# Kernel tuning notes

Measured on AMD Instinct MI355X. Metric: run time of the kernel, lower is better.

## Reference

```python
import jax, jax.numpy as jnp
import numpy as np

B, M, C, D, FF, FEAT = 1, 1024, 128, 512, 1024, 20
PAIR = 3 * D + 2 * FEAT  # slow_scorer_size = 1576


def _ffnn(x, W0, b0, W1, b1):
    # FFNN(depth=1): hidden relu layer then linear output (eval mode, no dropout)
    return jax.nn.relu(x @ W0 + b0) @ W1 + b1


def _batch_gather(x, idx):
    # x: [B, M, ...], idx: [B, ...] int -> gather along mention dim per batch
    return jax.vmap(lambda xb, ib: xb[ib])(x, idx)


def _bucket_distance(d):
    # log-scale distance buckets 0..9 (identity for d<=4)
    log_idx = jnp.floor(jnp.log(jnp.maximum(d, 1).astype(jnp.float32)) / jnp.log(2.0)).astype(jnp.int32) + 3
    return jnp.clip(jnp.where(d <= 4, d, log_idx), 0, 9)


def setup_inputs() -> dict:
    key = jax.random.key(0)
    ks = jax.random.split(key, 10)
    s = 0.02
    return {
        'mention_emb': jax.random.normal(ks[0], (B, M, D), dtype=jnp.float32),
        'mention_cluster_ids': jax.random.randint(ks[1], (B, M), 0, 200),
        'mention_speaker_ids': jax.random.randint(ks[2], (B, M), 0, 2),
        'ms_W0': jax.random.normal(ks[3], (D, FF), dtype=jnp.float32) * s,
        'ms_b0': jnp.zeros((FF,), jnp.float32),
        'ms_W1': jax.random.normal(ks[4], (FF, 1), dtype=jnp.float32) * s,
        'ms_b1': jnp.zeros((1,), jnp.float32),
        'sp_W0': jax.random.normal(ks[5], (PAIR, FF), dtype=jnp.float32) * s,
        'sp_b0': jnp.zeros((FF,), jnp.float32),
        'sp_W1': jax.random.normal(ks[6], (FF, 1), dtype=jnp.float32) * s,
        'sp_b1': jnp.zeros((1,), jnp.float32),
        'speaker_emb': jax.random.normal(ks[7], (2, FEAT), dtype=jnp.float32) * s,
        'bucket_emb': jax.random.normal(ks[8], (10, FEAT), dtype=jnp.float32) * s,
    }


def reference(mention_emb, mention_cluster_ids, mention_speaker_ids,
              ms_W0, ms_b0, ms_W1, ms_b1,
              sp_W0, sp_b0, sp_W1, sp_b1,
              speaker_emb, bucket_emb):
    # mention scoring
    mention_scores = _ffnn(mention_emb, ms_W0, ms_b0, ms_W1, ms_b1)[..., 0]  # [B, M]

    # get_antecedent_info: fixed window of C previous mentions
    offsets = jnp.arange(1, C + 1)[None, None, :]                    # [1,1,C]
    raw = jnp.arange(M)[None, :, None] - offsets                      # [1,M,C]
    antecedents = jnp.broadcast_to(jnp.clip(raw, 0, M - 1), (B, M, C))
    ant_mask = jnp.broadcast_to(raw >= 0, (B, M, C))

    fast_scores = _batch_gather(mention_scores, antecedents) + mention_scores[:, :, None]
    antecedent_emb = _batch_gather(mention_emb, antecedents)          # [B,M,C,D]

    # slow pair scorer features
    same_speaker = (_batch_gather(mention_speaker_ids, antecedents) == mention_speaker_ids[:, :, None]).astype(jnp.int32)
    speaker_feat = speaker_emb[same_speaker]                          # [B,M,C,FEAT]
    bucket_feat = jnp.broadcast_to(bucket_emb[_bucket_distance(offsets)], (B, M, C, FEAT))

    src = jnp.broadcast_to(mention_emb[:, :, None, :], (B, M, C, D))
    pair_emb = jnp.concatenate([src, antecedent_emb, src * antecedent_emb, speaker_feat, bucket_feat], axis=-1)
    slow_scores = _ffnn(pair_emb, sp_W0, sp_b0, sp_W1, sp_b1)[..., 0]  # [B,M,C]

    antecedent_scores = fast_scores + slow_scores + jnp.log(ant_mask.astype(jnp.float32))
    overall_scores = jnp.concatenate([jnp.zeros((B, M, 1), jnp.float32), antecedent_scores], axis=2)
    overall_dist = jax.nn.softmax(overall_scores, axis=-1)
    eps = 1e-6
    overall_dist = jnp.clip(overall_dist, eps, 1.0 - eps)
    overall_dist = overall_dist / jnp.sum(overall_dist, axis=-1, keepdims=True)

    # coref loss from cluster ids
    ant_cluster = _batch_gather(mention_cluster_ids, antecedents) * ant_mask.astype(mention_cluster_ids.dtype)
    same_cluster = ant_cluster == mention_cluster_ids[:, :, None]
    non_dummy = (mention_cluster_ids > 0)[:, :, None]
    ant_labels = same_cluster & non_dummy
    dummy_labels = ~jnp.any(ant_labels, axis=2, keepdims=True)
    overall_labels = jnp.concatenate([dummy_labels, ant_labels], axis=2)
    loss = -jnp.sum(jnp.log(overall_dist) * overall_labels.astype(jnp.float32), axis=2)
    loss = jnp.mean(jnp.sum(loss, axis=1))
    return overall_dist, loss
```

## Files before the change

kernel.cpp:

```cpp
#include <hip/hip_runtime.h>
#include <math.h>

#define MM 1024
#define DD 512
#define CC 128
#define LDSR 516


typedef __attribute__((ext_vector_type(8))) short bf16x8;
typedef __attribute__((ext_vector_type(4), aligned(8))) short bf16x4a;
typedef __attribute__((ext_vector_type(4))) float f32x4;
typedef __attribute__((ext_vector_type(16))) float f32x16;

__device__ __forceinline__ ushort bf16_rn(float x) {
    uint u = __float_as_uint(x);
    uint r = u + 0x7fffu + ((u >> 16) & 1u);
    return (ushort)(r >> 16);
}
__device__ __forceinline__ float bf16_to_f(ushort u) {
    return __uint_as_float(((uint)u) << 16);
}
__device__ __forceinline__ bf16x8 ld_lds16(const ushort* p) {
    bf16x4a lo = *(const bf16x4a*)p;
    bf16x4a hi = *(const bf16x4a*)(p + 4);
    return __builtin_shufflevector(lo, hi, 0, 1, 2, 3, 4, 5, 6, 7);
}

__global__ __launch_bounds__(256) void prep_emb(const float* __restrict__ emb,
                                                ushort* __restrict__ embb)
{
    int i = blockIdx.x * 256 + threadIdx.x;
    float2 v = ((const float2*)emb)[i];
    ushort2 o;
    o.x = bf16_rn(v.x);
    o.y = bf16_rn(v.y);
    ((ushort2*)embb)[i] = o;
}

__global__ __launch_bounds__(256) void prep_wall(const float* __restrict__ ms_W0,
                                                 const float* __restrict__ sp_W0,
                                                 ushort* __restrict__ Wall)
{
    __shared__ float t[64][65];
    const int k0 = blockIdx.x * 64;
    const int n0 = blockIdx.y * 64;
    const int g = n0 >> 10;
    const float* src = (g == 0) ? ms_W0 : (sp_W0 + (size_t)(g - 1) * 512 * 1024);
    const int col0 = n0 & 1023;
    const int tr = threadIdx.x >> 6, tc = threadIdx.x & 63;
#pragma unroll
    for (int i = 0; i < 16; ++i) {
        int k = tr + i * 4;
        t[k][tc] = src[(size_t)(k0 + k) * 1024 + col0 + tc];
    }
    __syncthreads();
    const int f = threadIdx.x >> 2;
    const int c4 = threadIdx.x & 3;
    ushort tmp[16];
#pragma unroll
    for (int j = 0; j < 16; ++j) tmp[j] = bf16_rn(t[c4 * 16 + j][f]);
    uint4* dst = (uint4*)(Wall + (size_t)(n0 + f) * 512 + k0 + c4 * 16);
    dst[0] = *(uint4*)&tmp[0];
    dst[1] = *(uint4*)&tmp[8];
}

__global__ __launch_bounds__(64) void prep_wfrag(const float* __restrict__ sp_W0,
                                                 ushort* __restrict__ Wfrag)
{
    const int ts = blockIdx.x;
    const int l = threadIdx.x;
    const int tt = ts >> 5, s = ts & 31;
    const int f = tt * 32 + (l & 31);
    const int kb = s * 16 + (l >> 5) * 8;
    const float* W = sp_W0 + (size_t)1024 * 1024;
    ushort tmp[8];
#pragma unroll
    for (int j = 0; j < 8; ++j) tmp[j] = bf16_rn(W[(size_t)(kb + j) * 1024 + f]);
    uint4* dst = (uint4*)(Wfrag + ((size_t)ts * 64 + l) * 8);
    *dst = *(uint4*)&tmp[0];
}

__global__ __launch_bounds__(256) void gemm_h_mfma(
    const ushort* __restrict__ embb, const ushort* __restrict__ Wall,
    float* __restrict__ H)
{
    const int n0 = blockIdx.x * 128;
    const int m0 = blockIdx.y * 128;
    const int lane = threadIdx.x & 63, wave = threadIdx.x >> 6;
    const int wx = wave & 1, wy = wave >> 1;
    const int l15 = lane & 15, lq = lane >> 4;

    const ushort* arow[4];
#pragma unroll
    for (int mi = 0; mi < 4; ++mi)
        arow[mi] = embb + (size_t)(m0 + wy * 64 + mi * 16 + l15) * 512;
    const ushort* brow[4];
#pragma unroll
    for (int ni = 0; ni < 4; ++ni)
        brow[ni] = Wall + (size_t)(n0 + wx * 64 + ni * 16 + l15) * 512;

    f32x4 acc[4][4];
#pragma unroll
    for (int i = 0; i < 4; ++i)
#pragma unroll
        for (int j = 0; j < 4; ++j) acc[i][j] = (f32x4)0.f;

    for (int kt = 0; kt < 512; kt += 32) {
        const int ko = kt + lq * 8;
        bf16x8 av[4], bv[4];
#pragma unroll
        for (int mi = 0; mi < 4; ++mi) av[mi] = *(const bf16x8*)(arow[mi] + ko);
#pragma unroll
        for (int ni = 0; ni < 4; ++ni) bv[ni] = *(const bf16x8*)(brow[ni] + ko);
#pragma unroll
        for (int mi = 0; mi < 4; ++mi)
#pragma unroll
            for (int ni = 0; ni < 4; ++ni)
                acc[mi][ni] = __builtin_amdgcn_mfma_f32_16x16x32_bf16(av[mi], bv[ni], acc[mi][ni], 0, 0, 0);
    }
#pragma unroll
    for (int mi = 0; mi < 4; ++mi)
#pragma unroll
        for (int r = 0; r < 4; ++r) {
            int mrow = m0 + wy * 64 + mi * 16 + lq * 4 + r;
#pragma unroll
            for (int ni = 0; ni < 4; ++ni)
                H[(size_t)mrow * 3072 + n0 + wx * 64 + ni * 16 + l15] = acc[mi][ni][r];
        }
}

__global__ void small_proj(const float* __restrict__ speaker_emb,
                           const float* __restrict__ bucket_emb,
                           const float* __restrict__ sp_W0,
                           float* __restrict__ spk_proj, float* __restrict__ bkt_proj)
{
    int r = blockIdx.x;
    const float* e; const float* W; float* out;
    if (r < 2) { e = speaker_emb + r * 20; W = sp_W0 + (size_t)1536 * 1024; out = spk_proj + r * 1024; }
    else       { e = bucket_emb + (r - 2) * 20; W = sp_W0 + (size_t)1556 * 1024; out = bkt_proj + (r - 2) * 1024; }
    float ek[20];
#pragma unroll
    for (int k = 0; k < 20; ++k) ek[k] = e[k];
    for (int f = threadIdx.x; f < 1024; f += blockDim.x) {
        float s = 0.f;
#pragma unroll
        for (int k = 0; k < 20; ++k) s = fmaf(ek[k], W[(size_t)k * 1024 + f], s);
        out[f] = s;
    }
}

__global__ __launch_bounds__(256) void mention_score(
    const float* __restrict__ H, const float* __restrict__ ms_b0,
    const float* __restrict__ ms_W1, const float* __restrict__ ms_b1,
    float* __restrict__ ms)
{
    int m = blockIdx.x;
    float v = 0.f;
    for (int f = threadIdx.x; f < 1024; f += 256) {
        float h = H[(size_t)m * 3072 + f] + ms_b0[f];
        v += fmaxf(h, 0.f) * ms_W1[f];
    }
#pragma unroll
    for (int o = 1; o < 64; o <<= 1) v += __shfl_xor(v, o);
    __shared__ float sm[4];
    if ((threadIdx.x & 63) == 0) sm[threadIdx.x >> 6] = v;
    __syncthreads();
    if (threadIdx.x == 0) ms[m] = sm[0] + sm[1] + sm[2] + sm[3] + ms_b1[0];
}

template<int CHALF>
__global__ __launch_bounds__(512, 4) void pair_mfma(
    const ushort* __restrict__ embb, const ushort* __restrict__ Wfrag,
    const float* __restrict__ H, const float* __restrict__ spk_proj,
    const float* __restrict__ bkt_proj, const float* __restrict__ sp_b0,
    const float* __restrict__ sp_W1, const int* __restrict__ speaker,
    float* __restrict__ slow)
{
    extern __shared__ ushort Alds[];
    float* red = (float*)(Alds + 64 * LDSR);
    int* meta_ss = (int*)(red + 8 * 64);
    int* meta_bk = meta_ss + 64;
    const int m = blockIdx.x;
    const int fh = blockIdx.y;
    const int cbase = CHALF * 64;
    const int tid = threadIdx.x;
    const int spk_m = speaker[m];

    {
        const int c = tid >> 3;
        const int kh = (tid & 7) * 64;
        int a = m - 1 - (cbase + c); if (a < 0) a = 0;
        const ushort* ea = embb + (size_t)a * 512 + kh;
        const ushort* em = embb + (size_t)m * 512 + kh;
        ushort* dst = Alds + c * LDSR + kh;
#pragma unroll
        for (int j = 0; j < 64; j += 8) {
            bf16x8 va = *(const bf16x8*)(ea + j);
            bf16x8 vm = *(const bf16x8*)(em + j);
            uint pr[4];
#pragma unroll
            for (int p = 0; p < 4; ++p) {
                float q0 = bf16_to_f((ushort)va[2 * p])     * bf16_to_f((ushort)vm[2 * p]);
                float q1 = bf16_to_f((ushort)va[2 * p + 1]) * bf16_to_f((ushort)vm[2 * p + 1]);
                pr[p] = __builtin_amdgcn_perm(__float_as_uint(q1), __float_as_uint(q0), 0x07060302u);
            }
            *(uint2*)(dst + j)     = *(uint2*)&pr[0];
            *(uint2*)(dst + j + 4) = *(uint2*)&pr[2];
        }
        if ((tid & 7) == 0) {
            meta_ss[c] = (speaker[a] == spk_m) ? 1 : 0;
            if (CHALF == 0) {
                int off = c + 1;
                int bk;
                if (off <= 4) bk = off;
                else { bk = 31 - __clz(off) + 3; if (bk > 9) bk = 9; }
                meta_bk[c] = bk;
            }
        }
    }
    __syncthreads();

    const int lane = tid & 63;
    const int wave = __builtin_amdgcn_readfirstlane(tid >> 6);
    const int l31 = lane & 31, k5 = lane >> 5;

    const int f0 = fh * 512 + wave * 64;
    const ushort* bb = Wfrag + (size_t)(fh * 16 + wave * 2) * 16384 + (size_t)lane * 8;
    const ushort* ab = Alds + l31 * LDSR + k5 * 8;

    f32x16 acc[2][2];
#pragma unroll
    for (int i = 0; i < 2; ++i)
#pragma unroll
        for (int j = 0; j < 2; ++j) acc[i][j] = (f32x16)0.f;

#pragma unroll 2
    for (int s = 0; s < 32; ++s) {
        bf16x8 b0 = *(const bf16x8*)(bb + s * 512);
        bf16x8 b1 = *(const bf16x8*)(bb + 16384 + s * 512);
        bf16x8 a0 = ld_lds16(ab + s * 16);
        bf16x8 a1 = ld_lds16(ab + 32 * LDSR + s * 16);
        acc[0][0] = __builtin_amdgcn_mfma_f32_32x32x16_bf16(a0, b0, acc[0][0], 0, 0, 0);
        acc[0][1] = __builtin_amdgcn_mfma_f32_32x32x16_bf16(a0, b1, acc[0][1], 0, 0, 0);
        acc[1][0] = __builtin_amdgcn_mfma_f32_32x32x16_bf16(a1, b0, acc[1][0], 0, 0, 0);
        acc[1][1] = __builtin_amdgcn_mfma_f32_32x32x16_bf16(a1, b1, acc[1][1], 0, 0, 0);
    }

    float srcb[2], w1v[2], sp0v[2], sp1v[2], bk9v[2];
#pragma unroll
    for (int ni = 0; ni < 2; ++ni) {
        int fcol = f0 + ni * 32 + l31;
        srcb[ni] = H[(size_t)m * 3072 + 1024 + fcol] + sp_b0[fcol];
        w1v[ni]  = sp_W1[fcol];
        sp0v[ni] = spk_proj[fcol];
        sp1v[ni] = spk_proj[1024 + fcol];
        if (CHALF == 1) bk9v[ni] = bkt_proj[9 * 1024 + fcol];
    }
#pragma unroll
    for (int mi = 0; mi < 2; ++mi) {
#pragma unroll
        for (int reg = 0; reg < 16; ++reg) {
            const int c = mi * 32 + 4 * k5 + (reg & 3) + 8 * (reg >> 2);
            int a = m - 1 - (cbase + c); if (a < 0) a = 0;
            const int ss = meta_ss[c];
            const float* antp = H + (size_t)a * 3072 + 2048;
            float s = 0.f;
#pragma unroll
            for (int ni = 0; ni < 2; ++ni) {
                const int fcol = f0 + ni * 32 + l31;
                float bval = (CHALF == 1) ? bk9v[ni]
                                          : bkt_proj[(size_t)meta_bk[c] * 1024 + fcol];
                float pre = acc[mi][ni][reg] + srcb[ni] + antp[fcol] + (ss ? sp1v[ni] : sp0v[ni]) + bval;
                s += fmaxf(pre, 0.f) * w1v[ni];
            }
            s += __shfl_xor(s, 1); s += __shfl_xor(s, 2); s += __shfl_xor(s, 4);
            s += __shfl_xor(s, 8); s += __shfl_xor(s, 16);
            if (l31 == 0) red[wave * 64 + c] = s;
        }
    }
    __syncthreads();
    if (tid < 64) {
        float s = 0.f;
#pragma unroll
        for (int i = 0; i < 8; ++i) s += red[i * 64 + tid];
        atomicAdd(slow + (size_t)m * 128 + cbase + tid, s);
    }
}

__device__ __forceinline__ float bsum2(float v, float* sm) {
#pragma unroll
    for (int o = 1; o < 64; o <<= 1) v += __shfl_xor(v, o);
    __syncthreads();
    if ((threadIdx.x & 63) == 0) sm[threadIdx.x >> 6] = v;
    __syncthreads();
    return sm[0] + sm[1];
}
__device__ __forceinline__ float bmax2(float v, float* sm) {
#pragma unroll
    for (int o = 1; o < 64; o <<= 1) v = fmaxf(v, __shfl_xor(v, o));
    __syncthreads();
    if ((threadIdx.x & 63) == 0) sm[threadIdx.x >> 6] = v;
    __syncthreads();
    return fmaxf(sm[0], sm[1]);
}

__global__ __launch_bounds__(128) void softmax_loss(
    const float* __restrict__ slow, const float* __restrict__ ms,
    const float* __restrict__ sp_b1, const int* __restrict__ cluster,
    float* __restrict__ out, float* __restrict__ loss_partial)
{
    const int m = blockIdx.x, c = threadIdx.x;
    __shared__ float sm[2];
    const int raw = m - 1 - c;
    const bool maskv = raw >= 0;
    const int a = maskv ? raw : 0;
    float score = slow[(size_t)m * 128 + c] + sp_b1[0] + ms[m] + ms[a];
    if (!maskv) score = -INFINITY;

    float mx = fmaxf(bmax2(score, sm), 0.f);
    float e = expf(score - mx);
    float e0 = expf(0.f - mx);
    float sum = bsum2(e, sm) + e0;
    float p = e / sum, p0 = e0 / sum;
    const float eps = 1e-6f;
    p  = fminf(fmaxf(p,  eps), 1.f - eps);
    p0 = fminf(fmaxf(p0, eps), 1.f - eps);
    float sum2 = bsum2(p, sm) + p0;
    p /= sum2; p0 /= sum2;
    out[(size_t)m * 129 + 1 + c] = p;
    if (c == 0) out[(size_t)m * 129] = p0;

    const int cid = cluster[m];
    const bool lbl = maskv && (cid > 0) && (cluster[a] == cid);
    float anyc = bsum2(lbl ? 1.f : 0.f, sm);
    float lsum = bsum2(lbl ? -logf(p) : 0.f, sm);
    if (c == 0) {
        if (anyc == 0.f) lsum += -logf(p0);
        loss_partial[m] = lsum;
    }
}

__global__ void loss_sum(const float* __restrict__ lp, float* __restrict__ out) {
    float v = 0.f;
    for (int i = threadIdx.x; i < 1024; i += 256) v += lp[i];
#pragma unroll
    for (int o = 1; o < 64; o <<= 1) v += __shfl_xor(v, o);
    __shared__ float sm[4];
    if ((threadIdx.x & 63) == 0) sm[threadIdx.x >> 6] = v;
    __syncthreads();
    if (threadIdx.x == 0) out[(size_t)1024 * 129] = sm[0] + sm[1] + sm[2] + sm[3];
}

extern "C" void kernel_launch(void* const* d_in, const int* in_sizes, int n_in,
                              void* d_out, int out_size, void* d_ws, size_t ws_size,
                              hipStream_t stream)
{
    const float* emb   = (const float*)d_in[0];
    const int*   clus  = (const int*)  d_in[1];
    const int*   spk   = (const int*)  d_in[2];
    const float* ms_W0 = (const float*)d_in[3];
    const float* ms_b0 = (const float*)d_in[4];
    const float* ms_W1 = (const float*)d_in[5];
    const float* ms_b1 = (const float*)d_in[6];
    const float* sp_W0 = (const float*)d_in[7];
    const float* sp_b0 = (const float*)d_in[8];
    const float* sp_W1 = (const float*)d_in[9];
    const float* sp_b1 = (const float*)d_in[10];
    const float* spke  = (const float*)d_in[11];
    const float* bkte  = (const float*)d_in[12];

    float* ws = (float*)d_ws;
    float* H        = ws;
    float* slow     = ws + 3145728;
    float* spk_proj = ws + 3276800;
    float* bkt_proj = ws + 3278848;
    float* msc      = ws + 3289088;
    float* lossp    = ws + 3290112;
    ushort* embb    = (ushort*)(ws + 3291136);
    ushort* Wall    = (ushort*)(ws + 3553280);
    ushort* Wfrag   = Wall + (size_t)3072 * 512;
    float* out = (float*)d_out;

    const int pair_lds = 64 * LDSR * 2 + 8 * 64 * 4 + 2 * 64 * 4;

    static bool attr_set = false;
    if (!attr_set) {
        hipFuncSetAttribute((const void*)&pair_mfma<0>,
                            hipFuncAttributeMaxDynamicSharedMemorySize,
                            pair_lds);
        hipFuncSetAttribute((const void*)&pair_mfma<1>,
                            hipFuncAttributeMaxDynamicSharedMemorySize,
                            pair_lds);
        attr_set = true;
    }

    hipMemsetAsync(slow, 0, (size_t)1024 * 128 * sizeof(float), stream);
    hipLaunchKernelGGL(prep_emb, dim3(1024), dim3(256), 0, stream, emb, embb);
    hipLaunchKernelGGL(prep_wall, dim3(8, 48), dim3(256), 0, stream, ms_W0, sp_W0, Wall);
    hipLaunchKernelGGL(prep_wfrag, dim3(1024), dim3(64), 0, stream, sp_W0, Wfrag);
    hipLaunchKernelGGL(gemm_h_mfma, dim3(24, 8), dim3(256), 0, stream, embb, Wall, H);
    hipLaunchKernelGGL(small_proj, dim3(12), dim3(256), 0, stream, spke, bkte, sp_W0, spk_proj, bkt_proj);
    hipLaunchKernelGGL(mention_score, dim3(1024), dim3(256), 0, stream, H, ms_b0, ms_W1, ms_b1, msc);
    hipLaunchKernelGGL(HIP_KERNEL_NAME(pair_mfma<0>), dim3(1024, 2), dim3(512), pair_lds, stream,
                       embb, Wfrag, H, spk_proj, bkt_proj, sp_b0, sp_W1, spk, slow);
    hipLaunchKernelGGL(HIP_KERNEL_NAME(pair_mfma<1>), dim3(1024, 2), dim3(512), pair_lds, stream,
                       embb, Wfrag, H, spk_proj, bkt_proj, sp_b0, sp_W1, spk, slow);
    hipLaunchKernelGGL(softmax_loss, dim3(1024), dim3(128), 0, stream,
                       slow, msc, sp_b1, clus, out, lossp);
    hipLaunchKernelGGL(loss_sum, dim3(1), dim3(256), 0, stream, lossp, out);
}
```

Before: 382.5 us.

## Compute antecedent projection inside pair kernel instead of gathering precomputed H rows

The antecedent-embedding part of the pair hidden layer was previously precomputed per mention in the big H GEMM and then gathered per pair. It is now computed directly in the pair kernel as a second MFMA pass over the antecedent embeddings staged in LDS. This shrinks the H GEMM from 3072 to 2048 output columns and drops scattered fp32 gathers in the epilogue. In exchange the pair kernel does twice the MFMA work and adds a second weight-fragment prep and extra LDS reloads and barriers. The two template launches are also merged into one launch with a 4-wide grid.

New measurement: 477.5 us. 24.8% more time.

```diff
diff --git a/kernel.cpp b/kernel.cpp
--- a/kernel.cpp
+++ b/kernel.cpp
@@ -64,19 +64,18 @@
     dst[1] = *(uint4*)&tmp[8];
 }
 
-__global__ __launch_bounds__(64) void prep_wfrag(const float* __restrict__ sp_W0,
-                                                 ushort* __restrict__ Wfrag)
+__global__ __launch_bounds__(64) void prep_wfrag(const float* __restrict__ W,
+                                                 ushort* __restrict__ dst_frag)
 {
     const int ts = blockIdx.x;
     const int l = threadIdx.x;
     const int tt = ts >> 5, s = ts & 31;
     const int f = tt * 32 + (l & 31);
     const int kb = s * 16 + (l >> 5) * 8;
-    const float* W = sp_W0 + (size_t)1024 * 1024;
     ushort tmp[8];
 #pragma unroll
     for (int j = 0; j < 8; ++j) tmp[j] = bf16_rn(W[(size_t)(kb + j) * 1024 + f]);
-    uint4* dst = (uint4*)(Wfrag + ((size_t)ts * 64 + l) * 8);
+    uint4* dst = (uint4*)(dst_frag + ((size_t)ts * 64 + l) * 8);
     *dst = *(uint4*)&tmp[0];
 }
 
@@ -168,9 +167,9 @@
     if (threadIdx.x == 0) ms[m] = sm[0] + sm[1] + sm[2] + sm[3] + ms_b1[0];
 }
 
-template<int CHALF>
 __global__ __launch_bounds__(512, 4) void pair_mfma(
     const ushort* __restrict__ embb, const ushort* __restrict__ Wfrag,
+    const ushort* __restrict__ WfragAnt,
     const float* __restrict__ H, const float* __restrict__ spk_proj,
     const float* __restrict__ bkt_proj, const float* __restrict__ sp_b0,
     const float* __restrict__ sp_W1, const int* __restrict__ speaker,
@@ -181,21 +180,22 @@
     int* meta_ss = (int*)(red + 8 * 64);
     int* meta_bk = meta_ss + 64;
     const int m = blockIdx.x;
-    const int fh = blockIdx.y;
-    const int cbase = CHALF * 64;
+    const int cbase = (blockIdx.y & 1) * 64;
+    const int fh = blockIdx.y >> 1;
     const int tid = threadIdx.x;
     const int spk_m = speaker[m];
 
+    const int cA = tid >> 3;
+    const int khA = (tid & 7) * 64;
+    int aA = m - 1 - (cbase + cA); if (aA < 0) aA = 0;
+    const ushort* eaA = embb + (size_t)aA * 512 + khA;
+    ushort* dstA = Alds + cA * LDSR + khA;
+
     {
-        const int c = tid >> 3;
-        const int kh = (tid & 7) * 64;
-        int a = m - 1 - (cbase + c); if (a < 0) a = 0;
-        const ushort* ea = embb + (size_t)a * 512 + kh;
-        const ushort* em = embb + (size_t)m * 512 + kh;
-        ushort* dst = Alds + c * LDSR + kh;
+        const ushort* em = embb + (size_t)m * 512 + khA;
 #pragma unroll
         for (int j = 0; j < 64; j += 8) {
-            bf16x8 va = *(const bf16x8*)(ea + j);
+            bf16x8 va = *(const bf16x8*)(eaA + j);
             bf16x8 vm = *(const bf16x8*)(em + j);
             uint pr[4];
 #pragma unroll
@@ -204,18 +204,16 @@
                 float q1 = bf16_to_f((ushort)va[2 * p + 1]) * bf16_to_f((ushort)vm[2 * p + 1]);
                 pr[p] = __builtin_amdgcn_perm(__float_as_uint(q1), __float_as_uint(q0), 0x07060302u);
             }
-            *(uint2*)(dst + j)     = *(uint2*)&pr[0];
-            *(uint2*)(dst + j + 4) = *(uint2*)&pr[2];
+            *(uint2*)(dstA + j)     = *(uint2*)&pr[0];
+            *(uint2*)(dstA + j + 4) = *(uint2*)&pr[2];
         }
         if ((tid & 7) == 0) {
-            meta_ss[c] = (speaker[a] == spk_m) ? 1 : 0;
-            if (CHALF == 0) {
-                int off = c + 1;
-                int bk;
-                if (off <= 4) bk = off;
-                else { bk = 31 - __clz(off) + 3; if (bk > 9) bk = 9; }
-                meta_bk[c] = bk;
-            }
+            meta_ss[cA] = (speaker[aA] == spk_m) ? 1 : 0;
+            int off = cbase + cA + 1;
+            int bk;
+            if (off <= 4) bk = off;
+            else { bk = 31 - __clz(off) + 3; if (bk > 9) bk = 9; }
+            meta_bk[cA] = bk;
         }
     }
     __syncthreads();
@@ -223,30 +221,60 @@
     const int lane = tid & 63;
     const int wave = __builtin_amdgcn_readfirstlane(tid >> 6);
     const int l31 = lane & 31, k5 = lane >> 5;
+    const ushort* ab = Alds + l31 * LDSR + k5 * 8;
+
+    f32x16 acc[2][2];
+#pragma unroll
+    for (int i = 0; i < 2; ++i)
+#pragma unroll
+        for (int j = 0; j < 2; ++j) acc[i][j] = (f32x16)0.f;
+
+    {
+        const ushort* bb = Wfrag + (size_t)(fh * 16 + wave * 2) * 16384 + (size_t)lane * 8;
+#pragma unroll 2
+        for (int s = 0; s < 32; ++s) {
+            bf16x8 b0 = *(const bf16x8*)(bb + s * 512);
+            bf16x8 b1 = *(const bf16x8*)(bb + 16384 + s * 512);
+            bf16x8 a0 = ld_lds16(ab + s * 16);
+            bf16x8 a1 = ld_lds16(ab + 32 * LDSR + s * 16);
+            acc[0][0] = __builtin_amdgcn_mfma_f32_32x32x16_bf16(a0, b0, acc[0][0], 0, 0, 0);
+            acc[0][1] = __builtin_amdgcn_mfma_f32_32x32x16_bf16(a0, b1, acc[0][1], 0, 0, 0);
+            acc[1][0] = __builtin_amdgcn_mfma_f32_32x32x16_bf16(a1, b0, acc[1][0], 0, 0, 0);
+            acc[1][1] = __builtin_amdgcn_mfma_f32_32x32x16_bf16(a1, b1, acc[1][1], 0, 0, 0);
+        }
+    }
+    __syncthreads();
+
+    {
+#pragma unroll
+        for (int j = 0; j < 64; j += 16) {
+            bf16x8 v0 = *(const bf16x8*)(eaA + j);
+            bf16x8 v1 = *(const bf16x8*)(eaA + j + 8);
+            *(uint2*)(dstA + j)      = *(uint2*)&v0;
+            *(uint2*)(dstA + j + 4)  = *((uint2*)&v0 + 1);
+            *(uint2*)(dstA + j + 8)  = *(uint2*)&v1;
+            *(uint2*)(dstA + j + 12) = *((uint2*)&v1 + 1);
+        }
+    }
+    __syncthreads();
+
+    {
+        const ushort* bb = WfragAnt + (size_t)(fh * 16 + wave * 2) * 16384 + (size_t)lane * 8;
+#pragma unroll 2
+        for (int s = 0; s < 32; ++s) {
+            bf16x8 b0 = *(const bf16x8*)(bb + s * 512);
+            bf16x8 b1 = *(const bf16x8*)(bb + 16384 + s * 512);
+            bf16x8 a0 = ld_lds16(ab + s * 16);
+            bf16x8 a1 = ld_lds16(ab + 32 * LDSR + s * 16);
+            acc[0][0] = __builtin_amdgcn_mfma_f32_32x32x16_bf16(a0, b0, acc[0][0], 0, 0, 0);
+            acc[0][1] = __builtin_amdgcn_mfma_f32_32x32x16_bf16(a0, b1, acc[0][1], 0, 0, 0);
+            acc[1][0] = __builtin_amdgcn_mfma_f32_32x32x16_bf16(a1, b0, acc[1][0], 0, 0, 0);
+            acc[1][1] = __builtin_amdgcn_mfma_f32_32x32x16_bf16(a1, b1, acc[1][1], 0, 0, 0);
+        }
+    }
 
     const int f0 = fh * 512 + wave * 64;
-    const ushort* bb = Wfrag + (size_t)(fh * 16 + wave * 2) * 16384 + (size_t)lane * 8;
-    const ushort* ab = Alds + l31 * LDSR + k5 * 8;
-
-    f32x16 acc[2][2];
-#pragma unroll
-    for (int i = 0; i < 2; ++i)
-#pragma unroll
-        for (int j = 0; j < 2; ++j) acc[i][j] = (f32x16)0.f;
-
-#pragma unroll 2
-    for (int s = 0; s < 32; ++s) {
-        bf16x8 b0 = *(const bf16x8*)(bb + s * 512);
-        bf16x8 b1 = *(const bf16x8*)(bb + 16384 + s * 512);
-        bf16x8 a0 = ld_lds16(ab + s * 16);
-        bf16x8 a1 = ld_lds16(ab + 32 * LDSR + s * 16);
-        acc[0][0] = __builtin_amdgcn_mfma_f32_32x32x16_bf16(a0, b0, acc[0][0], 0, 0, 0);
-        acc[0][1] = __builtin_amdgcn_mfma_f32_32x32x16_bf16(a0, b1, acc[0][1], 0, 0, 0);
-        acc[1][0] = __builtin_amdgcn_mfma_f32_32x32x16_bf16(a1, b0, acc[1][0], 0, 0, 0);
-        acc[1][1] = __builtin_amdgcn_mfma_f32_32x32x16_bf16(a1, b1, acc[1][1], 0, 0, 0);
-    }
-
-    float srcb[2], w1v[2], sp0v[2], sp1v[2], bk9v[2];
+    float srcb[2], w1v[2], sp0v[2], sp1v[2];
 #pragma unroll
     for (int ni = 0; ni < 2; ++ni) {
         int fcol = f0 + ni * 32 + l31;
@@ -254,23 +282,20 @@
         w1v[ni]  = sp_W1[fcol];
         sp0v[ni] = spk_proj[fcol];
         sp1v[ni] = spk_proj[1024 + fcol];
-        if (CHALF == 1) bk9v[ni] = bkt_proj[9 * 1024 + fcol];
     }
 #pragma unroll
     for (int mi = 0; mi < 2; ++mi) {
 #pragma unroll
         for (int reg = 0; reg < 16; ++reg) {
             const int c = mi * 32 + 4 * k5 + (reg & 3) + 8 * (reg >> 2);
-            int a = m - 1 - (cbase + c); if (a < 0) a = 0;
             const int ss = meta_ss[c];
-            const float* antp = H + (size_t)a * 3072 + 2048;
+            const int bk = meta_bk[c];
             float s = 0.f;
 #pragma unroll
             for (int ni = 0; ni < 2; ++ni) {
                 const int fcol = f0 + ni * 32 + l31;
-                float bval = (CHALF == 1) ? bk9v[ni]
-                                          : bkt_proj[(size_t)meta_bk[c] * 1024 + fcol];
-                float pre = acc[mi][ni][reg] + srcb[ni] + antp[fcol] + (ss ? sp1v[ni] : sp0v[ni]) + bval;
+                float bval = bkt_proj[(size_t)bk * 1024 + fcol];
+                float pre = acc[mi][ni][reg] + srcb[ni] + (ss ? sp1v[ni] : sp0v[ni]) + bval;
                 s += fmaxf(pre, 0.f) * w1v[ni];
             }
             s += __shfl_xor(s, 1); s += __shfl_xor(s, 2); s += __shfl_xor(s, 4);
@@ -378,6 +403,7 @@
     float* lossp    = ws + 3290112;
     ushort* embb    = (ushort*)(ws + 3291136);
     ushort* Wall    = (ushort*)(ws + 3553280);
+    ushort* WfragAnt= Wall + (size_t)2048 * 512;
     ushort* Wfrag   = Wall + (size_t)3072 * 512;
     float* out = (float*)d_out;
 
@@ -385,10 +411,7 @@
 
     static bool attr_set = false;
     if (!attr_set) {
-        hipFuncSetAttribute((const void*)&pair_mfma<0>,
-                            hipFuncAttributeMaxDynamicSharedMemorySize,
-                            pair_lds);
-        hipFuncSetAttribute((const void*)&pair_mfma<1>,
+        hipFuncSetAttribute((const void*)&pair_mfma,
                             hipFuncAttributeMaxDynamicSharedMemorySize,
                             pair_lds);
         attr_set = true;
@@ -396,15 +419,16 @@
 
     hipMemsetAsync(slow, 0, (size_t)1024 * 128 * sizeof(float), stream);
     hipLaunchKernelGGL(prep_emb, dim3(1024), dim3(256), 0, stream, emb, embb);
-    hipLaunchKernelGGL(prep_wall, dim3(8, 48), dim3(256), 0, stream, ms_W0, sp_W0, Wall);
-    hipLaunchKernelGGL(prep_wfrag, dim3(1024), dim3(64), 0, stream, sp_W0, Wfrag);
-    hipLaunchKernelGGL(gemm_h_mfma, dim3(24, 8), dim3(256), 0, stream, embb, Wall, H);
+    hipLaunchKernelGGL(prep_wall, dim3(8, 32), dim3(256), 0, stream, ms_W0, sp_W0, Wall);
+    hipLaunchKernelGGL(prep_wfrag, dim3(1024), dim3(64), 0, stream,
+                       sp_W0 + (size_t)1024 * 1024, Wfrag);
+    hipLaunchKernelGGL(prep_wfrag, dim3(1024), dim3(64), 0, stream,
+                       sp_W0 + (size_t)512 * 1024, WfragAnt);
+    hipLaunchKernelGGL(gemm_h_mfma, dim3(16, 8), dim3(256), 0, stream, embb, Wall, H);
     hipLaunchKernelGGL(small_proj, dim3(12), dim3(256), 0, stream, spke, bkte, sp_W0, spk_proj, bkt_proj);
     hipLaunchKernelGGL(mention_score, dim3(1024), dim3(256), 0, stream, H, ms_b0, ms_W1, ms_b1, msc);
-    hipLaunchKernelGGL(HIP_KERNEL_NAME(pair_mfma<0>), dim3(1024, 2), dim3(512), pair_lds, stream,
-                       embb, Wfrag, H, spk_proj, bkt_proj, sp_b0, sp_W1, spk, slow);
-    hipLaunchKernelGGL(HIP_KERNEL_NAME(pair_mfma<1>), dim3(1024, 2), dim3(512), pair_lds, stream,
-                       embb, Wfrag, H, spk_proj, bkt_proj, sp_b0, sp_W1, spk, slow);
+    hipLaunchKernelGGL(pair_mfma, dim3(1024, 4), dim3(512), pair_lds, stream,
+                       embb, Wfrag, WfragAnt, H, spk_proj, bkt_proj, sp_b0, sp_W1, spk, slow);
     hipLaunchKernelGGL(softmax_loss, dim3(1024), dim3(128), 0, stream,
                        slow, msc, sp_b1, clus, out, lossp);
     hipLaunchKernelGGL(loss_sum, dim3(1), dim3(256), 0, stream, lossp, out);
```
